# Kernel optimization log

Measured on AMD Instinct MI355X. Metric: run time of the kernel, lower is better.

The kernel has to match this reference:

```python
import jax, jax.numpy as jnp
import numpy as np

LN_EPS = 1e-5

def _ln(x, g, b):
    # LayerNorm over last dim; torch normalized_shape=[1,H] on [B,1,H] reduces to this
    mu = jnp.mean(x, axis=-1, keepdims=True)
    var = jnp.var(x, axis=-1, keepdims=True)
    return (x - mu) * jax.lax.rsqrt(var + LN_EPS) * g + b


def setup_inputs() -> dict:
    key = jax.random.key(0)
    B, T, D, H = 32, 2048, 512, 128
    ks = jax.random.split(key, 10)
    stdu = 1.0 / np.sqrt(H)
    u = lambda k, sh: jax.random.uniform(k, sh, jnp.float32, -stdu, stdu)
    return {
        "x": jax.random.normal(ks[0], (B, T, D), jnp.float32),
        "W_f": u(ks[1], (D, H)), "W_i": u(ks[2], (D, H)),
        "W_o": u(ks[3], (D, H)), "W_c": u(ks[4], (D, H)),
        "U_f": u(ks[5], (H, H)), "U_i": u(ks[6], (H, H)),
        "U_o": u(ks[7], (H, H)), "U_c": u(ks[8], (H, H)),
        "b_f": jnp.ones((H,), jnp.float32),
        "b_i": jnp.zeros((H,), jnp.float32),
        "b_o": jnp.zeros((H,), jnp.float32),
        "b_c": jnp.zeros((H,), jnp.float32),
        "ln_f_g": jnp.ones((H,), jnp.float32), "ln_f_b": jnp.zeros((H,), jnp.float32),
        "ln_i_g": jnp.ones((H,), jnp.float32), "ln_i_b": jnp.zeros((H,), jnp.float32),
        "ln_o_g": jnp.ones((H,), jnp.float32), "ln_o_b": jnp.zeros((H,), jnp.float32),
        "ln_c_g": jnp.ones((H,), jnp.float32), "ln_c_b": jnp.zeros((H,), jnp.float32),
        "h0": jnp.zeros((B, H), jnp.float32),
        "c0": jnp.zeros((B, H), jnp.float32),
        "zoneout_mask": jax.random.randint(ks[9], (T,), 0, 2, jnp.int32),
    }


def reference(x, W_f, W_i, W_o, W_c, U_f, U_i, U_o, U_c,
              b_f, b_i, b_o, b_c,
              ln_f_g, ln_f_b, ln_i_g, ln_i_b, ln_o_g, ln_o_b, ln_c_g, ln_c_b,
              h0, c0, zoneout_mask):
    xs = jnp.swapaxes(x, 0, 1)                       # [T, B, D]
    m = zoneout_mask.astype(x.dtype)[:, None, None]  # [T, 1, 1] zoneout indicator

    def step(carry, inp):
        h, c = carry
        x_t, mt = inp
        f = jax.nn.sigmoid(_ln(x_t @ W_f + h @ U_f + b_f, ln_f_g, ln_f_b))
        i = jax.nn.sigmoid(_ln(x_t @ W_i + h @ U_i + b_i, ln_i_g, ln_i_b))
        o = jax.nn.sigmoid(_ln(x_t @ W_o + h @ U_o + b_o, ln_o_g, ln_o_b))
        ch = jax.nn.sigmoid(_ln(x_t @ W_c + h @ U_c + b_c, ln_c_g, ln_c_b))
        c_new = mt * c + (1.0 - mt) * (f * c + i * ch)
        # NOTE: source applies sigmoid (not tanh) to the cell state
        h_new = mt * h + (1.0 - mt) * (o * jax.nn.sigmoid(c_new))
        return (h_new, c_new), h_new

    (h_T, c_T), out_seq = jax.lax.scan(step, (h0, c0), (xs, m))
    return jnp.swapaxes(out_seq, 0, 1), h_T          # [B, T, H], [B, H]
```

## Files before the change

kernel.cpp:

```cpp
#include <hip/hip_runtime.h>
#include <hip/hip_bf16.h>

#define Bx 32
#define Tt 2048
#define Dd 512
#define Hh 128
#define APS 152
#define PROW 520
#define SGS 528

typedef __attribute__((ext_vector_type(8))) short short8;
typedef __attribute__((ext_vector_type(4))) float f32x4;

static __device__ __forceinline__ short f2bf(float f) {
    __hip_bfloat16 h = __float2bfloat16(f);
    return *reinterpret_cast<short*>(&h);
}
static __device__ __forceinline__ float sigm(float x) {
    return 1.f / (1.f + __expf(-x));
}
static __device__ __forceinline__ float swz_xor16_add(float v) {
    return v + __int_as_float(__builtin_amdgcn_ds_swizzle(__float_as_int(v), 0x401F));
}

#define BARRIER_LGKM() asm volatile("s_waitcnt lgkmcnt(0)\n\ts_barrier" ::: "memory")

typedef __attribute__((address_space(1))) const void gas_void;
typedef __attribute__((address_space(3))) void las_void;
static __device__ __forceinline__ void gl_lds16(const float* g, float* l) {
    __builtin_amdgcn_global_load_lds((gas_void*)g, (las_void*)l, 16, 0, 0);
}

__global__ __launch_bounds__(512, 2) void gemm_xw_mfma(
    const float* __restrict__ X,
    const float* __restrict__ W0, const float* __restrict__ W1,
    const float* __restrict__ W2, const float* __restrict__ W3,
    const float* __restrict__ B0, const float* __restrict__ B1,
    const float* __restrict__ B2, const float* __restrict__ B3,
    float* __restrict__ G)
{
    __shared__ __align__(16) short As[128][40];
    __shared__ __align__(16) short Bs[512][40];

    const int tid  = threadIdx.x;
    const int m0   = blockIdx.x * 128;
    const int lane = tid & 63;
    const int w    = tid >> 6;
    const int wr   = w >> 2, wc = w & 3;
    const int l15  = lane & 15, kb = lane >> 4;

    const int bn   = tid;
    const int gate = bn >> 7;
    const int j    = bn & 127;
    const float* __restrict__ Wg = (gate == 0) ? W0 : (gate == 1) ? W1 : (gate == 2) ? W2 : W3;

    const int am = tid >> 2;
    const int ak = (tid & 3) * 8;

    const float* __restrict__ Bg = (wc == 0) ? B0 : (wc == 1) ? B1 : (wc == 2) ? B2 : B3;
    f32x4 acc[4][8];
    #pragma unroll
    for (int nt = 0; nt < 8; ++nt) {
        const float bv = Bg[nt * 16 + l15];
        #pragma unroll
        for (int mt = 0; mt < 4; ++mt)
            acc[mt][nt] = (f32x4){bv, bv, bv, bv};
    }

    for (int k0 = 0; k0 < Dd; k0 += 32) {
        {
            const float4* xp = (const float4*)&X[(size_t)(m0 + am) * Dd + k0 + ak];
            float4 v0 = xp[0], v1 = xp[1];
            short8 s;
            s[0] = f2bf(v0.x); s[1] = f2bf(v0.y); s[2] = f2bf(v0.z); s[3] = f2bf(v0.w);
            s[4] = f2bf(v1.x); s[5] = f2bf(v1.y); s[6] = f2bf(v1.z); s[7] = f2bf(v1.w);
            *(short8*)&As[am][ak] = s;
        }
        #pragma unroll
        for (int rc = 0; rc < 4; ++rc) {
            float v[8];
            #pragma unroll
            for (int r = 0; r < 8; ++r)
                v[r] = Wg[(size_t)(k0 + rc * 8 + r) * Hh + j];
            short8 s;
            #pragma unroll
            for (int r = 0; r < 8; ++r) s[r] = f2bf(v[r]);
            *(short8*)&Bs[bn][rc * 8] = s;
        }
        __syncthreads();

        short8 a[4], b[8];
        #pragma unroll
        for (int mt = 0; mt < 4; ++mt)
            a[mt] = *(const short8*)&As[wr * 64 + mt * 16 + l15][kb * 8];
        #pragma unroll
        for (int nt = 0; nt < 8; ++nt)
            b[nt] = *(const short8*)&Bs[wc * 128 + nt * 16 + l15][kb * 8];
        #pragma unroll
        for (int mt = 0; mt < 4; ++mt)
            #pragma unroll
            for (int nt = 0; nt < 8; ++nt)
                acc[mt][nt] = __builtin_amdgcn_mfma_f32_16x16x32_bf16(a[mt], b[nt], acc[mt][nt], 0, 0, 0);
        __syncthreads();
    }

    #pragma unroll
    for (int mt = 0; mt < 4; ++mt)
        #pragma unroll
        for (int nt = 0; nt < 8; ++nt)
            #pragma unroll
            for (int r = 0; r < 4; ++r)
                G[(size_t)(m0 + wr * 64 + mt * 16 + kb * 4 + r) * 512 + wc * 128 + nt * 16 + l15]
                    = acc[mt][nt][r];
}

__global__ __launch_bounds__(256, 1) void lstm_scan_mfma(
    const float* __restrict__ G,
    const float* __restrict__ Uf, const float* __restrict__ Ui,
    const float* __restrict__ Uo, const float* __restrict__ Uc,
    const float* __restrict__ lnfg, const float* __restrict__ lnfb,
    const float* __restrict__ lnig, const float* __restrict__ lnib,
    const float* __restrict__ lnog, const float* __restrict__ lnob,
    const float* __restrict__ lncg, const float* __restrict__ lncb,
    const float* __restrict__ h0, const float* __restrict__ c0,
    const int* __restrict__ zmask,
    float* __restrict__ out, float* __restrict__ hT)
{
    const int tid  = threadIdx.x;
    const int lane = tid & 63;
    const int w    = tid >> 6;
    const int b0   = blockIdx.x * 4;
    const int l15  = lane & 15;
    const int kb   = lane >> 4;

    __shared__ __align__(16) short Ap[16 * APS];
    __shared__ __align__(16) float SLN[4 * SGS];
    __shared__ __align__(16) float Pan[2 * 4 * 4 * PROW];
    __shared__ unsigned short act[Tt];
    __shared__ int wsum[4], wpre[4];
    __shared__ int nact_sh;

    const float* __restrict__ Ug = (w == 0) ? Uf : (w == 1) ? Ui : (w == 2) ? Uo : Uc;
    short8 bfr[8][4];
    #pragma unroll
    for (int nt = 0; nt < 8; ++nt) {
        #pragma unroll
        for (int ks = 0; ks < 4; ++ks) {
            short8 v;
            #pragma unroll
            for (int r = 0; r < 8; ++r)
                v[r] = f2bf(Ug[(ks * 32 + kb * 8 + r) * Hh + nt * 16 + l15]);
            bfr[nt][ks] = v;
        }
    }

    const int j1 = lane, j2 = lane + 64;
    const float gF1 = lnfg[j1], bF1 = lnfb[j1], gF2 = lnfg[j2], bF2 = lnfb[j2];
    const float gI1 = lnig[j1], bI1 = lnib[j1], gI2 = lnig[j2], bI2 = lnib[j2];
    const float gO1 = lnog[j1], bO1 = lnob[j1], gO2 = lnog[j2], bO2 = lnob[j2];
    const float gC1 = lncg[j1], bC1 = lncb[j1], gC2 = lncg[j2], bC2 = lncb[j2];

    float hv0 = h0[(b0 + w) * Hh + j1];
    float hv1 = h0[(b0 + w) * Hh + j2];
    float cv0 = c0[(b0 + w) * Hh + j1];
    float cv1 = c0[(b0 + w) * Hh + j2];

    for (int i = tid; i < 16 * APS; i += 256) Ap[i] = 0;
    __syncthreads();
    Ap[w * APS + j1] = f2bf(hv0);
    Ap[w * APS + j2] = f2bf(hv1);

    {
        const int base_t = tid * 8;
        int fl[8], cnt = 0;
        #pragma unroll
        for (int i = 0; i < 8; ++i) { fl[i] = (zmask[base_t + i] == 0); cnt += fl[i]; }
        int scan = cnt;
        #pragma unroll
        for (int off = 1; off <= 32; off <<= 1) {
            int v = __shfl_up(scan, off);
            if (lane >= off) scan += v;
        }
        if (lane == 63) wsum[w] = scan;
        __syncthreads();
        if (tid == 0) {
            int s = 0;
            #pragma unroll
            for (int i = 0; i < 4; ++i) { wpre[i] = s; s += wsum[i]; }
            nact_sh = s;
        }
        __syncthreads();
        int pos = wpre[w] + scan - cnt;
        #pragma unroll
        for (int i = 0; i < 8; ++i)
            if (fl[i]) act[pos++] = (unsigned short)(base_t + i);
    }
    __syncthreads();
    const int nact = nact_sh;

    const int firstA = (nact > 0) ? (int)act[0] : Tt;
    for (int tt = 0; tt < firstA; ++tt) {
        out[((size_t)(b0 + w) * Tt + tt) * Hh + j1] = hv0;
        out[((size_t)(b0 + w) * Tt + tt) * Hh + j2] = hv1;
    }

    auto stage_panel = [&](int kp, int buf) {
        #pragma unroll
        for (int si = 0; si < 4; ++si) {
            const int s    = w * 4 + si;
            const int slot = s >> 2;
            const int bb   = s & 3;
            const int kidx = kp + slot;
            if (kidx < nact) {
                const int tt = (int)act[kidx];
                const float* src = &G[((size_t)(b0 + bb) * Tt + tt) * 512];
                float* dst = &Pan[((buf * 4 + slot) * 4 + bb) * PROW];
                gl_lds16(src + lane * 4, dst);
                gl_lds16(src + 256 + lane * 4, dst + 256);
            }
        }
    };

    int cur = 0;
    stage_panel(0, 0);
    asm volatile("s_waitcnt vmcnt(0)" ::: "memory");
    __syncthreads();

    const int lb = l15 & 3;

    auto lstm_step = [&](int kidx, int slot) {
        const int t_ = (int)act[kidx];

        short8 a0 = *(const short8*)&Ap[l15 * APS +  0 + kb * 8];
        short8 a1 = *(const short8*)&Ap[l15 * APS + 32 + kb * 8];
        short8 a2 = *(const short8*)&Ap[l15 * APS + 64 + kb * 8];
        short8 a3 = *(const short8*)&Ap[l15 * APS + 96 + kb * 8];

        const int pbase = ((cur * 4 + slot) * 4 + lb) * PROW + w * 128 + kb * 4;
        f32x4 Cv[8];
        #pragma unroll
        for (int nt = 0; nt < 8; ++nt)
            Cv[nt] = *(const f32x4*)&Pan[pbase + nt * 16];

        #pragma unroll
        for (int nt = 0; nt < 8; ++nt)
            Cv[nt] = __builtin_amdgcn_mfma_f32_16x16x32_bf16(bfr[nt][0], a0, Cv[nt], 0, 0, 0);
        #pragma unroll
        for (int nt = 0; nt < 8; ++nt)
            Cv[nt] = __builtin_amdgcn_mfma_f32_16x16x32_bf16(bfr[nt][1], a1, Cv[nt], 0, 0, 0);
        #pragma unroll
        for (int nt = 0; nt < 8; ++nt)
            Cv[nt] = __builtin_amdgcn_mfma_f32_16x16x32_bf16(bfr[nt][2], a2, Cv[nt], 0, 0, 0);
        #pragma unroll
        for (int nt = 0; nt < 8; ++nt)
            Cv[nt] = __builtin_amdgcn_mfma_f32_16x16x32_bf16(bfr[nt][3], a3, Cv[nt], 0, 0, 0);

        float sm = 0.f, sq = 0.f;
        #pragma unroll
        for (int nt = 0; nt < 8; ++nt)
            #pragma unroll
            for (int r = 0; r < 4; ++r) {
                sm += Cv[nt][r];
                sq = fmaf(Cv[nt][r], Cv[nt][r], sq);
            }
        sm = swz_xor16_add(sm);
        sq = swz_xor16_add(sq);
        sm += __shfl_xor(sm, 32);
        sq += __shfl_xor(sq, 32);
        const float mu   = sm * (1.f / 128.f);
        const float rstd = rsqrtf(sq * (1.f / 128.f) - mu * mu + 1e-5f);
        const float na = rstd, nc = -mu * rstd;
        #pragma unroll
        for (int nt = 0; nt < 8; ++nt)
            #pragma unroll
            for (int r = 0; r < 4; ++r)
                Cv[nt][r] = fmaf(Cv[nt][r], na, nc);

        if (l15 < 4) {
            #pragma unroll
            for (int nt = 0; nt < 8; ++nt)
                *(f32x4*)&SLN[w * SGS + l15 * 132 + nt * 16 + kb * 4] = Cv[nt];
        }
        BARRIER_LGKM();

        {
            const int sb = w * 132;
            const float nf0 = SLN[0 * SGS + sb + j1], nf1 = SLN[0 * SGS + sb + j2];
            const float ni0 = SLN[1 * SGS + sb + j1], ni1 = SLN[1 * SGS + sb + j2];
            const float no0 = SLN[2 * SGS + sb + j1], no1 = SLN[2 * SGS + sb + j2];
            const float nc0 = SLN[3 * SGS + sb + j1], nc1 = SLN[3 * SGS + sb + j2];
            const float f0 = sigm(fmaf(nf0, gF1, bF1));
            const float i0 = sigm(fmaf(ni0, gI1, bI1));
            const float o0 = sigm(fmaf(no0, gO1, bO1));
            const float g0 = sigm(fmaf(nc0, gC1, bC1));
            const float f1 = sigm(fmaf(nf1, gF2, bF2));
            const float i1 = sigm(fmaf(ni1, gI2, bI2));
            const float o1 = sigm(fmaf(no1, gO2, bO2));
            const float g1 = sigm(fmaf(nc1, gC2, bC2));
            cv0 = f0 * cv0 + i0 * g0;
            hv0 = o0 * sigm(cv0);
            cv1 = f1 * cv1 + i1 * g1;
            hv1 = o1 * sigm(cv1);
            Ap[w * APS + j1] = f2bf(hv0);
            Ap[w * APS + j2] = f2bf(hv1);
            out[((size_t)(b0 + w) * Tt + t_) * Hh + j1] = hv0;
            out[((size_t)(b0 + w) * Tt + t_) * Hh + j2] = hv1;
        }
        BARRIER_LGKM();
    };

    for (int kp = 0; kp < nact; kp += 4) {
        stage_panel(kp + 4, cur ^ 1);
        const int lim = (nact - kp < 4) ? (nact - kp) : 4;
        #pragma unroll
        for (int sl = 0; sl < 4; ++sl) {
            if (sl < lim) {
                lstm_step(kp + sl, sl);
                if (sl == 3)
                    asm volatile("s_waitcnt vmcnt(0)" ::: "memory");
            }
        }
        cur ^= 1;
    }

    hT[(b0 + w) * Hh + j1] = hv0;
    hT[(b0 + w) * Hh + j2] = hv1;
}

__global__ __launch_bounds__(512) void fill_zoneout(
    const int* __restrict__ zmask, const float* __restrict__ h0,
    float* __restrict__ out)
{
    const int t = blockIdx.x;
    if (zmask[t] == 0) return;
    int s = t - 1;
    while (s >= 0 && zmask[s] != 0) --s;
    const int tid = threadIdx.x;
    for (int idx = tid; idx < Bx * Hh; idx += 512) {
        const int b = idx >> 7, j = idx & 127;
        const float v = (s >= 0) ? out[((size_t)b * Tt + s) * Hh + j]
                                 : h0[b * Hh + j];
        out[((size_t)b * Tt + t) * Hh + j] = v;
    }
}

extern "C" void kernel_launch(void* const* d_in, const int* in_sizes, int n_in,
                              void* d_out, int out_size, void* d_ws, size_t ws_size,
                              hipStream_t stream)
{
    const float* x   = (const float*)d_in[0];
    const float* W_f = (const float*)d_in[1];
    const float* W_i = (const float*)d_in[2];
    const float* W_o = (const float*)d_in[3];
    const float* W_c = (const float*)d_in[4];
    const float* U_f = (const float*)d_in[5];
    const float* U_i = (const float*)d_in[6];
    const float* U_o = (const float*)d_in[7];
    const float* U_c = (const float*)d_in[8];
    const float* b_f = (const float*)d_in[9];
    const float* b_i = (const float*)d_in[10];
    const float* b_o = (const float*)d_in[11];
    const float* b_c = (const float*)d_in[12];
    const float* ln_f_g = (const float*)d_in[13];
    const float* ln_f_b = (const float*)d_in[14];
    const float* ln_i_g = (const float*)d_in[15];
    const float* ln_i_b = (const float*)d_in[16];
    const float* ln_o_g = (const float*)d_in[17];
    const float* ln_o_b = (const float*)d_in[18];
    const float* ln_c_g = (const float*)d_in[19];
    const float* ln_c_b = (const float*)d_in[20];
    const float* h0  = (const float*)d_in[21];
    const float* c0  = (const float*)d_in[22];
    const int*   zm  = (const int*)d_in[23];

    float* out = (float*)d_out;
    float* hT  = out + (size_t)Bx * Tt * Hh;
    float* G   = (float*)d_ws;

    gemm_xw_mfma<<<(Bx * Tt) / 128, 512, 0, stream>>>(x, W_f, W_i, W_o, W_c,
                                                      b_f, b_i, b_o, b_c, G);

    lstm_scan_mfma<<<8, 256, 0, stream>>>(G, U_f, U_i, U_o, U_c,
                                          ln_f_g, ln_f_b, ln_i_g, ln_i_b,
                                          ln_o_g, ln_o_b, ln_c_g, ln_c_b,
                                          h0, c0, zm, out, hT);

    fill_zoneout<<<Tt, 512, 0, stream>>>(zm, h0, out);
}
```

Baseline: 1.614 ms.

## Split scan block into two 2-batch wave groups with 512 threads

The recurrent scan kernel now runs 8 waves per block instead of 4. The waves form two independent groups, each handling 2 of the block's 4 batch rows, with separate h buffers, LN staging and G panels in shared memory. Each lane now computes one hidden unit instead of two, which halves the per-thread elementwise and sigmoid work per step and doubles wave-level parallelism on the serial critical path. The trade-off is that both groups still run the full 16-row MFMA with half the rows idle, and block-wide barriers now sync 8 waves per step.

After: 2.016 ms. 1.25x slower.

```diff
diff --git a/kernel.cpp b/kernel.cpp
--- a/kernel.cpp
+++ b/kernel.cpp
@@ -7,7 +7,6 @@
 #define Hh 128
 #define APS 152
 #define PROW 520
-#define SGS 528
 
 typedef __attribute__((ext_vector_type(8))) short short8;
 typedef __attribute__((ext_vector_type(4))) float f32x4;
@@ -114,7 +113,7 @@
                     = acc[mt][nt][r];
 }
 
-__global__ __launch_bounds__(256, 1) void lstm_scan_mfma(
+__global__ __launch_bounds__(512, 2) void lstm_scan_mfma(
     const float* __restrict__ G,
     const float* __restrict__ Uf, const float* __restrict__ Ui,
     const float* __restrict__ Uo, const float* __restrict__ Uc,
@@ -129,18 +128,24 @@
     const int tid  = threadIdx.x;
     const int lane = tid & 63;
     const int w    = tid >> 6;
+    const int ch   = w >> 2;
+    const int wc   = w & 3;
     const int b0   = blockIdx.x * 4;
+    const int cb0  = b0 + ch * 2;
     const int l15  = lane & 15;
     const int kb   = lane >> 4;
-
-    __shared__ __align__(16) short Ap[16 * APS];
-    __shared__ __align__(16) float SLN[4 * SGS];
-    __shared__ __align__(16) float Pan[2 * 4 * 4 * PROW];
+    const int lb   = l15 & 1;
+
+    __shared__ __align__(16) short Ap[2][16 * APS];
+    __shared__ __align__(16) float SLN[2][2][4][132];
+    __shared__ __align__(16) float Pan[2 * 2 * 4 * 2 * PROW];
     __shared__ unsigned short act[Tt];
-    __shared__ int wsum[4], wpre[4];
+    __shared__ int wsum[8], wpre[8];
     __shared__ int nact_sh;
 
-    const float* __restrict__ Ug = (w == 0) ? Uf : (w == 1) ? Ui : (w == 2) ? Uo : Uc;
+#define PIDX(buf, chq, slot, bb) (((((buf) * 2 + (chq)) * 4 + (slot)) * 2 + (bb)) * PROW)
+
+    const float* __restrict__ Ug = (wc == 0) ? Uf : (wc == 1) ? Ui : (wc == 2) ? Uo : Uc;
     short8 bfr[8][4];
     #pragma unroll
     for (int nt = 0; nt < 8; ++nt) {
@@ -154,27 +159,25 @@
         }
     }
 
-    const int j1 = lane, j2 = lane + 64;
-    const float gF1 = lnfg[j1], bF1 = lnfb[j1], gF2 = lnfg[j2], bF2 = lnfb[j2];
-    const float gI1 = lnig[j1], bI1 = lnib[j1], gI2 = lnig[j2], bI2 = lnib[j2];
-    const float gO1 = lnog[j1], bO1 = lnob[j1], gO2 = lnog[j2], bO2 = lnob[j2];
-    const float gC1 = lncg[j1], bC1 = lncb[j1], gC2 = lncg[j2], bC2 = lncb[j2];
-
-    float hv0 = h0[(b0 + w) * Hh + j1];
-    float hv1 = h0[(b0 + w) * Hh + j2];
-    float cv0 = c0[(b0 + w) * Hh + j1];
-    float cv1 = c0[(b0 + w) * Hh + j2];
-
-    for (int i = tid; i < 16 * APS; i += 256) Ap[i] = 0;
+    const int bq = wc >> 1;
+    const int oj = ((wc & 1) << 6) + lane;
+    const float gF = lnfg[oj], bF = lnfb[oj];
+    const float gI = lnig[oj], bI = lnib[oj];
+    const float gO = lnog[oj], bO = lnob[oj];
+    const float gC = lncg[oj], bC = lncb[oj];
+
+    float hv = h0[(cb0 + bq) * Hh + oj];
+    float cv = c0[(cb0 + bq) * Hh + oj];
+
+    for (int i = tid; i < 2 * 16 * APS; i += 512) ((short*)Ap)[i] = 0;
     __syncthreads();
-    Ap[w * APS + j1] = f2bf(hv0);
-    Ap[w * APS + j2] = f2bf(hv1);
+    Ap[ch][bq * APS + oj] = f2bf(hv);
 
     {
-        const int base_t = tid * 8;
-        int fl[8], cnt = 0;
-        #pragma unroll
-        for (int i = 0; i < 8; ++i) { fl[i] = (zmask[base_t + i] == 0); cnt += fl[i]; }
+        const int base_t = tid * 4;
+        const int f0 = (zmask[base_t] == 0), f1 = (zmask[base_t + 1] == 0);
+        const int f2 = (zmask[base_t + 2] == 0), f3 = (zmask[base_t + 3] == 0);
+        const int cnt = f0 + f1 + f2 + f3;
         int scan = cnt;
         #pragma unroll
         for (int off = 1; off <= 32; off <<= 1) {
@@ -186,35 +189,34 @@
         if (tid == 0) {
             int s = 0;
             #pragma unroll
-            for (int i = 0; i < 4; ++i) { wpre[i] = s; s += wsum[i]; }
+            for (int i = 0; i < 8; ++i) { wpre[i] = s; s += wsum[i]; }
             nact_sh = s;
         }
         __syncthreads();
         int pos = wpre[w] + scan - cnt;
-        #pragma unroll
-        for (int i = 0; i < 8; ++i)
-            if (fl[i]) act[pos++] = (unsigned short)(base_t + i);
+        if (f0) act[pos++] = (unsigned short)(base_t);
+        if (f1) act[pos++] = (unsigned short)(base_t + 1);
+        if (f2) act[pos++] = (unsigned short)(base_t + 2);
+        if (f3) act[pos++] = (unsigned short)(base_t + 3);
     }
     __syncthreads();
     const int nact = nact_sh;
 
     const int firstA = (nact > 0) ? (int)act[0] : Tt;
-    for (int tt = 0; tt < firstA; ++tt) {
-        out[((size_t)(b0 + w) * Tt + tt) * Hh + j1] = hv0;
-        out[((size_t)(b0 + w) * Tt + tt) * Hh + j2] = hv1;
-    }
+    for (int tt = 0; tt < firstA; ++tt)
+        out[((size_t)(cb0 + bq) * Tt + tt) * Hh + oj] = hv;
 
     auto stage_panel = [&](int kp, int buf) {
         #pragma unroll
-        for (int si = 0; si < 4; ++si) {
-            const int s    = w * 4 + si;
-            const int slot = s >> 2;
-            const int bb   = s & 3;
+        for (int si = 0; si < 2; ++si) {
+            const int s    = wc * 2 + si;
+            const int slot = s >> 1;
+            const int bb   = s & 1;
             const int kidx = kp + slot;
             if (kidx < nact) {
                 const int tt = (int)act[kidx];
-                const float* src = &G[((size_t)(b0 + bb) * Tt + tt) * 512];
-                float* dst = &Pan[((buf * 4 + slot) * 4 + bb) * PROW];
+                const float* src = &G[((size_t)(cb0 + bb) * Tt + tt) * 512];
+                float* dst = &Pan[PIDX(buf, ch, slot, bb)];
                 gl_lds16(src + lane * 4, dst);
                 gl_lds16(src + 256 + lane * 4, dst + 256);
             }
@@ -226,17 +228,15 @@
     asm volatile("s_waitcnt vmcnt(0)" ::: "memory");
     __syncthreads();
 
-    const int lb = l15 & 3;
-
     auto lstm_step = [&](int kidx, int slot) {
         const int t_ = (int)act[kidx];
 
-        short8 a0 = *(const short8*)&Ap[l15 * APS +  0 + kb * 8];
-        short8 a1 = *(const short8*)&Ap[l15 * APS + 32 + kb * 8];
-        short8 a2 = *(const short8*)&Ap[l15 * APS + 64 + kb * 8];
-        short8 a3 = *(const short8*)&Ap[l15 * APS + 96 + kb * 8];
-
-        const int pbase = ((cur * 4 + slot) * 4 + lb) * PROW + w * 128 + kb * 4;
+        short8 a0 = *(const short8*)&Ap[ch][l15 * APS +  0 + kb * 8];
+        short8 a1 = *(const short8*)&Ap[ch][l15 * APS + 32 + kb * 8];
+        short8 a2 = *(const short8*)&Ap[ch][l15 * APS + 64 + kb * 8];
+        short8 a3 = *(const short8*)&Ap[ch][l15 * APS + 96 + kb * 8];
+
+        const int pbase = PIDX(cur, ch, slot, lb) + wc * 128 + kb * 4;
         f32x4 Cv[8];
         #pragma unroll
         for (int nt = 0; nt < 8; ++nt)
@@ -276,35 +276,26 @@
             for (int r = 0; r < 4; ++r)
                 Cv[nt][r] = fmaf(Cv[nt][r], na, nc);
 
-        if (l15 < 4) {
+        if (l15 < 2) {
             #pragma unroll
             for (int nt = 0; nt < 8; ++nt)
-                *(f32x4*)&SLN[w * SGS + l15 * 132 + nt * 16 + kb * 4] = Cv[nt];
+                *(f32x4*)&SLN[ch][l15][wc][nt * 16 + kb * 4] = Cv[nt];
         }
         BARRIER_LGKM();
 
         {
-            const int sb = w * 132;
-            const float nf0 = SLN[0 * SGS + sb + j1], nf1 = SLN[0 * SGS + sb + j2];
-            const float ni0 = SLN[1 * SGS + sb + j1], ni1 = SLN[1 * SGS + sb + j2];
-            const float no0 = SLN[2 * SGS + sb + j1], no1 = SLN[2 * SGS + sb + j2];
-            const float nc0 = SLN[3 * SGS + sb + j1], nc1 = SLN[3 * SGS + sb + j2];
-            const float f0 = sigm(fmaf(nf0, gF1, bF1));
-            const float i0 = sigm(fmaf(ni0, gI1, bI1));
-            const float o0 = sigm(fmaf(no0, gO1, bO1));
-            const float g0 = sigm(fmaf(nc0, gC1, bC1));
-            const float f1 = sigm(fmaf(nf1, gF2, bF2));
-            const float i1 = sigm(fmaf(ni1, gI2, bI2));
-            const float o1 = sigm(fmaf(no1, gO2, bO2));
-            const float g1 = sigm(fmaf(nc1, gC2, bC2));
-            cv0 = f0 * cv0 + i0 * g0;
-            hv0 = o0 * sigm(cv0);
-            cv1 = f1 * cv1 + i1 * g1;
-            hv1 = o1 * sigm(cv1);
-            Ap[w * APS + j1] = f2bf(hv0);
-            Ap[w * APS + j2] = f2bf(hv1);
-            out[((size_t)(b0 + w) * Tt + t_) * Hh + j1] = hv0;
-            out[((size_t)(b0 + w) * Tt + t_) * Hh + j2] = hv1;
+            const float nf  = SLN[ch][bq][0][oj];
+            const float ni  = SLN[ch][bq][1][oj];
+            const float no_ = SLN[ch][bq][2][oj];
+            const float ng  = SLN[ch][bq][3][oj];
+            const float f_ = sigm(fmaf(nf,  gF, bF));
+            const float i_ = sigm(fmaf(ni,  gI, bI));
+            const float o_ = sigm(fmaf(no_, gO, bO));
+            const float g_ = sigm(fmaf(ng,  gC, bC));
+            cv = f_ * cv + i_ * g_;
+            hv = o_ * sigm(cv);
+            Ap[ch][bq * APS + oj] = f2bf(hv);
+            out[((size_t)(cb0 + bq) * Tt + t_) * Hh + oj] = hv;
         }
         BARRIER_LGKM();
     };
@@ -323,8 +314,8 @@
         cur ^= 1;
     }
 
-    hT[(b0 + w) * Hh + j1] = hv0;
-    hT[(b0 + w) * Hh + j2] = hv1;
+    hT[(cb0 + bq) * Hh + oj] = hv;
+#undef PIDX
 }
 
 __global__ __launch_bounds__(512) void fill_zoneout(
@@ -380,7 +371,7 @@
     gemm_xw_mfma<<<(Bx * Tt) / 128, 512, 0, stream>>>(x, W_f, W_i, W_o, W_c,
                                                       b_f, b_i, b_o, b_c, G);
 
-    lstm_scan_mfma<<<8, 256, 0, stream>>>(G, U_f, U_i, U_o, U_c,
+    lstm_scan_mfma<<<8, 512, 0, stream>>>(G, U_f, U_i, U_o, U_c,
                                           ln_f_g, ln_f_b, ln_i_g, ln_i_b,
                                           ln_o_g, ln_o_b, ln_c_g, ln_c_b,
                                           h0, c0, zm, out, hT);
```
